# Kernel optimization log

Measured on AMD Instinct MI355X. Metric: run time of the kernel, lower is better.

The kernel has to match this reference:

```python
import jax, jax.numpy as jnp
import numpy as np

D_MODEL = 1024
N_HEADS = 16
D_K = D_MODEL // N_HEADS
B, L = 2, 2048


def setup_inputs() -> dict:
    key = jax.random.key(0)
    ks = jax.random.split(key, 13)
    s = 0.02
    inp = {
        'query': jax.random.normal(ks[0], (B, L, D_MODEL), jnp.float32),
        'key': jax.random.normal(ks[1], (B, L, D_MODEL), jnp.float32),
        'value': jax.random.normal(ks[2], (B, L, D_MODEL), jnp.float32),
        'mask': jax.random.randint(ks[3], (1, 1, L, L), 0, 2).astype(bool),
        'W_q': jax.random.normal(ks[4], (D_MODEL, D_MODEL), jnp.float32) * s,
        'b_q': jnp.zeros((D_MODEL,), jnp.float32),
        'W_k': jax.random.normal(ks[5], (D_MODEL, D_MODEL), jnp.float32) * s,
        'b_k': jnp.zeros((D_MODEL,), jnp.float32),
        'W_v': jax.random.normal(ks[6], (D_MODEL, D_MODEL), jnp.float32) * s,
        'b_v': jnp.zeros((D_MODEL,), jnp.float32),
        'W_o': jax.random.normal(ks[7], (D_MODEL, D_MODEL), jnp.float32) * s,
        'b_o': jnp.zeros((D_MODEL,), jnp.float32),
    }
    return inp


def _split_heads(x):
    b, l, _ = x.shape
    return x.reshape(b, l, N_HEADS, D_K).transpose(0, 2, 1, 3)  # [B,H,L,dk]


def reference(query, key, value, mask, W_q, b_q, W_k, b_k, W_v, b_v, W_o, b_o):
    q = _split_heads(query @ W_q + b_q)
    k = _split_heads(key @ W_k + b_k)
    v = _split_heads(value @ W_v + b_v)
    # Unscaled attention logits [B,H,L,L] (NO 1/sqrt(dk))
    logits = jnp.einsum('bhqd,bhkd->bhqk', q, k)
    logits = jnp.where(mask, -jnp.inf, logits)
    w = jax.nn.softmax(logits, axis=-1)
    w = jnp.nan_to_num(w, nan=0.0)  # fully-masked rows -> zeros
    attended = jnp.einsum('bhqk,bhkd->bhqd', w, v)
    # dropout in eval mode = identity; combine heads
    out = attended.transpose(0, 2, 1, 3).reshape(B, L, D_MODEL)
    return out @ W_o + b_o
```

## Files before the change

### kernel.cpp

```cpp
#include <hip/hip_runtime.h>
#include <hip/hip_bf16.h>
#include <stdint.h>


typedef __bf16 bf16;
typedef __bf16 bf16x8 __attribute__((ext_vector_type(8)));
typedef float f32x4 __attribute__((ext_vector_type(4)));

#define AS1 __attribute__((address_space(1)))
#define AS3 __attribute__((address_space(3)))

__device__ __forceinline__ void g2l16(const void* g, void* l) {
    __builtin_amdgcn_global_load_lds((AS1 void*)g, (AS3 void*)l, 16, 0, 0);
}

__global__ __launch_bounds__(256) void cvt3_kernel(const float* __restrict__ a0,
                                                   const float* __restrict__ a1,
                                                   const float* __restrict__ a2,
                                                   bf16* o0, bf16* o1, bf16* o2) {
    int y = blockIdx.y;
    const float* in = (y == 0) ? a0 : (y == 1) ? a1 : a2;
    bf16* out = (y == 0) ? o0 : (y == 1) ? o1 : o2;
    int idx = blockIdx.x * 256 + threadIdx.x;
    float4 v = ((const float4*)in)[idx];
    __align__(8) bf16 o[4];
    o[0] = (bf16)v.x; o[1] = (bf16)v.y; o[2] = (bf16)v.z; o[3] = (bf16)v.w;
    *(uint2*)(out + (size_t)idx * 4) = *(const uint2*)o;
}

__global__ __launch_bounds__(256) void mdetect_kernel(const unsigned int* __restrict__ w,
                                                      int* __restrict__ flag) {
    int idx = blockIdx.x * 256 + threadIdx.x;
    unsigned v = w[idx];
    int f = 0;
    if (v == 0x3F800000u) f = 2;
    else if (v > 1u) f = 1;
    unsigned long long b1 = __ballot(f & 1);
    unsigned long long b2 = __ballot(f & 2);
    if ((threadIdx.x & 63) == 0) {
        int agg = (b1 ? 1 : 0) | (b2 ? 2 : 0);
        if (agg) atomicOr(flag, agg);
    }
}

__global__ __launch_bounds__(256) void mpack_kernel(const void* __restrict__ mask,
                                                    unsigned long long* __restrict__ mb,
                                                    const int* __restrict__ flag) {
    int idx = blockIdx.x * 256 + threadIdx.x;
    int f = *flag;
    bool v;
    if (f & 2)      v = ((const float*)mask)[idx] != 0.0f;
    else if (f & 1) v = ((const unsigned char*)mask)[idx] != 0;
    else            v = ((const int*)mask)[idx] != 0;
    unsigned long long b = __ballot(v);
    if ((threadIdx.x & 63) == 0) mb[idx >> 6] = b;
}

__global__ __launch_bounds__(256) void wtrans_kernel(const float* W0, const float* W1,
                                                     const float* W2, const float* W3,
                                                     bf16* T0, bf16* T1, bf16* T2, bf16* T3) {
    const float* W; bf16* T;
    int y = blockIdx.y;
    if (y == 0)      { W = W0; T = T0; }
    else if (y == 1) { W = W1; T = T1; }
    else if (y == 2) { W = W2; T = T2; }
    else             { W = W3; T = T3; }
    int tx = blockIdx.x & 15, ty = blockIdx.x >> 4;
    int n0 = tx * 64, k0 = ty * 64;
    __shared__ __align__(16) bf16 t[64 * 72];
    int tid = threadIdx.x;
    #pragma unroll
    for (int rr = 0; rr < 4; ++rr) {
        int idx = rr * 256 + tid;
        int r = idx >> 4, c4 = (idx & 15) * 4;
        float4 v = *(const float4*)(W + (size_t)(k0 + r) * 1024 + n0 + c4);
        __align__(8) bf16 o[4];
        o[0] = (bf16)v.x; o[1] = (bf16)v.y; o[2] = (bf16)v.z; o[3] = (bf16)v.w;
        *(uint2*)&t[r * 72 + c4] = *(const uint2*)o;
    }
    __syncthreads();
    #pragma unroll
    for (int rr = 0; rr < 2; ++rr) {
        int idx = rr * 256 + tid;
        int n = idx >> 3, kc = (idx & 7) * 8;
        __align__(16) bf16 o[8];
        #pragma unroll
        for (int j = 0; j < 8; ++j) o[j] = t[(kc + j) * 72 + n];
        *(uint4*)(T + (size_t)(n0 + n) * 1024 + k0 + kc) = *(const uint4*)o;
    }
}

template <int MODE>
__device__ __forceinline__ void gemm128_core(const bf16* __restrict__ A,
                                             const bf16* __restrict__ Bt,
                                             const float* __restrict__ bias,
                                             void* __restrict__ Out, int bm, int bn) {
    __shared__ __align__(16) bf16 la[128 * 32];
    __shared__ __align__(16) bf16 lb[128 * 32];
    int tid = threadIdx.x;
    int w = tid >> 6, lane = tid & 63;
    int quad = lane >> 4, col = lane & 15;
    int wm = w >> 1, wn = w & 1;
    int m0 = bm * 128, n0 = bn * 128;
    f32x4 acc[4][4];
    f32x4 z = {0.f, 0.f, 0.f, 0.f};
    #pragma unroll
    for (int i = 0; i < 4; ++i)
        #pragma unroll
        for (int j = 0; j < 4; ++j) acc[i][j] = z;
    int srow = lane >> 2;
    int skc = (lane & 3) * 8;
    for (int kt = 0; kt < 32; ++kt) {
        int kk = kt * 32;
        __syncthreads();
        #pragma unroll
        for (int rr = 0; rr < 2; ++rr) {
            int ch = rr * 4 + w;
            int row = ch * 16 + srow;
            g2l16(A + (size_t)(m0 + row) * 1024 + kk + skc, &la[ch * 512]);
            g2l16(Bt + (size_t)(n0 + row) * 1024 + kk + skc, &lb[ch * 512]);
        }
        __syncthreads();
        bf16x8 af[4], bfr[4];
        #pragma unroll
        for (int mt = 0; mt < 4; ++mt)
            af[mt] = *(const bf16x8*)&la[(wm * 64 + mt * 16 + col) * 32 + quad * 8];
        #pragma unroll
        for (int nt = 0; nt < 4; ++nt)
            bfr[nt] = *(const bf16x8*)&lb[(wn * 64 + nt * 16 + col) * 32 + quad * 8];
        #pragma unroll
        for (int mt = 0; mt < 4; ++mt)
            #pragma unroll
            for (int nt = 0; nt < 4; ++nt)
                acc[mt][nt] = __builtin_amdgcn_mfma_f32_16x16x32_bf16(
                    af[mt], bfr[nt], acc[mt][nt], 0, 0, 0);
    }
    float bia[4];
    #pragma unroll
    for (int nt = 0; nt < 4; ++nt) bia[nt] = bias[n0 + wn * 64 + nt * 16 + col];
    #pragma unroll
    for (int mt = 0; mt < 4; ++mt) {
        #pragma unroll
        for (int nt = 0; nt < 4; ++nt) {
            #pragma unroll
            for (int r = 0; r < 4; ++r) {
                int m = m0 + wm * 64 + mt * 16 + quad * 4 + r;
                int n = n0 + wn * 64 + nt * 16 + col;
                float v = acc[mt][nt][r] + bia[nt];
                if (MODE == 0) {
                    int b = m >> 11, l = m & 2047, h = n >> 6, d = n & 63;
                    ((bf16*)Out)[(((size_t)b * 16 + h) * 2048 + l) * 64 + d] = (bf16)v;
                } else if (MODE == 1) {
                    ((float*)Out)[(size_t)m * 1024 + n] = v;
                } else {
                    int b = m >> 11, l = m & 2047, h = n >> 6, d = n & 63;
                    ((bf16*)Out)[(((size_t)b * 16 + h) * 64 + d) * 2048 + l] = (bf16)v;
                }
            }
        }
    }
}

__global__ __launch_bounds__(256) void qk_kernel(
    const bf16* Xq, const bf16* Xk, const bf16* Wq, const bf16* Wk,
    const float* bq, const float* bk, bf16* Qh, bf16* Kh) {
    int y = blockIdx.y;
    const bf16* A = y ? Xk : Xq;
    const bf16* Bt = y ? Wk : Wq;
    const float* bi = y ? bk : bq;
    bf16* O = y ? Kh : Qh;
    gemm128_core<0>(A, Bt, bi, O, blockIdx.x >> 3, blockIdx.x & 7);
}

__global__ __launch_bounds__(256) void vproj_kernel(const bf16* Xv, const bf16* Wv,
                                                    const float* bv, bf16* Vt) {
    gemm128_core<2>(Xv, Wv, bv, Vt, blockIdx.x >> 3, blockIdx.x & 7);
}

__global__ __launch_bounds__(256) void ogemm_kernel(const bf16* A, const bf16* Wt,
                                                    const float* bias, float* Out) {
    gemm128_core<1>(A, Wt, bias, Out, blockIdx.x >> 3, blockIdx.x & 7);
}

__global__ __launch_bounds__(256) void attn_kernel(const bf16* __restrict__ Qh,
                                                   const bf16* __restrict__ Kh,
                                                   const bf16* __restrict__ Vt,
                                                   const unsigned long long* __restrict__ mb,
                                                   bf16* __restrict__ att) {
    int bh = blockIdx.x, qt = blockIdx.y;
    int b = bh >> 4, h = bh & 15;
    int q0 = qt * 64;
    __shared__ __align__(16) bf16 qs[64 * 64];
    __shared__ __align__(16) bf16 ks[64 * 64];
    __shared__ __align__(16) bf16 vs[64 * 64];
    __shared__ __align__(16) bf16 ps[4 * 16 * 72];
    int tid = threadIdx.x;
    int w = tid >> 6, lane = tid & 63;
    int quad = lane >> 4, col = lane & 15;
    int c7 = col & 7;
    int sr = lane >> 3;
    int sg = (lane & 7) ^ (sr & 7);
    int swz0 = (quad ^ c7) * 8;
    int swz1 = ((4 + quad) ^ c7) * 8;

    #pragma unroll
    for (int rr = 0; rr < 2; ++rr) {
        int ch = rr * 4 + w;
        int r = ch * 8 + sr;
        g2l16(Qh + ((size_t)bh * 2048 + q0 + r) * 64 + sg * 8, &qs[ch * 512]);
    }
    __syncthreads();
    bf16x8 aq[2];
    aq[0] = *(const bf16x8*)&qs[(w * 16 + col) * 64 + swz0];
    aq[1] = *(const bf16x8*)&qs[(w * 16 + col) * 64 + swz1];

    f32x4 O[4];
    f32x4 z = {0.f, 0.f, 0.f, 0.f};
    float rs[4] = {0.f, 0.f, 0.f, 0.f};
    #pragma unroll
    for (int dt = 0; dt < 4; ++dt) O[dt] = z;

    for (int kt = 0; kt < 32; ++kt) {
        __syncthreads();
        #pragma unroll
        for (int rr = 0; rr < 2; ++rr) {
            int ch = rr * 4 + w;
            int r = ch * 8 + sr;
            g2l16(Kh + ((size_t)bh * 2048 + kt * 64 + r) * 64 + sg * 8, &ks[ch * 512]);
            g2l16(Vt + ((size_t)bh * 64 + r) * 2048 + kt * 64 + sg * 8, &vs[ch * 512]);
        }
        __syncthreads();

        f32x4 s[4];
        #pragma unroll
        for (int nt = 0; nt < 4; ++nt) {
            s[nt] = z;
            bf16x8 bk0 = *(const bf16x8*)&ks[(nt * 16 + col) * 64 + swz0];
            s[nt] = __builtin_amdgcn_mfma_f32_16x16x32_bf16(aq[0], bk0, s[nt], 0, 0, 0);
            bf16x8 bk1 = *(const bf16x8*)&ks[(nt * 16 + col) * 64 + swz1];
            s[nt] = __builtin_amdgcn_mfma_f32_16x16x32_bf16(aq[1], bk1, s[nt], 0, 0, 0);
        }

        #pragma unroll
        for (int r = 0; r < 4; ++r) {
            unsigned long long t = mb[(size_t)(q0 + w * 16 + quad * 4 + r) * 32 + kt] >> col;
            #pragma unroll
            for (int nt = 0; nt < 4; ++nt) {
                float p = __expf(s[nt][r] - 12.0f);
                if ((t >> (nt * 16)) & 1ull) p = 0.0f;
                rs[r] += p;
                s[nt][r] = p;
            }
        }

        #pragma unroll
        for (int nt = 0; nt < 4; ++nt)
            #pragma unroll
            for (int r = 0; r < 4; ++r)
                ps[w * 1152 + (quad * 4 + r) * 72 + nt * 16 + col] = (bf16)s[nt][r];

        bf16x8 ap[2];
        ap[0] = *(const bf16x8*)&ps[w * 1152 + col * 72 + quad * 8];
        ap[1] = *(const bf16x8*)&ps[w * 1152 + col * 72 + 32 + quad * 8];
        #pragma unroll
        for (int dt = 0; dt < 4; ++dt) {
            bf16x8 bv0 = *(const bf16x8*)&vs[(dt * 16 + col) * 64 + swz0];
            O[dt] = __builtin_amdgcn_mfma_f32_16x16x32_bf16(ap[0], bv0, O[dt], 0, 0, 0);
            bf16x8 bv1 = *(const bf16x8*)&vs[(dt * 16 + col) * 64 + swz1];
            O[dt] = __builtin_amdgcn_mfma_f32_16x16x32_bf16(ap[1], bv1, O[dt], 0, 0, 0);
        }
    }

    #pragma unroll
    for (int r = 0; r < 4; ++r) {
        #pragma unroll
        for (int d = 1; d < 16; d <<= 1) rs[r] += __shfl_xor(rs[r], d);
    }

    #pragma unroll
    for (int r = 0; r < 4; ++r) {
        float inv = (rs[r] > 0.f) ? 1.0f / rs[r] : 0.f;
        int qg = q0 + w * 16 + quad * 4 + r;
        #pragma unroll
        for (int dt = 0; dt < 4; ++dt) {
            float ov = O[dt][r] * inv;
            att[((size_t)b * 2048 + qg) * 1024 + h * 64 + dt * 16 + col] = (bf16)ov;
        }
    }
}

extern "C" void kernel_launch(void* const* d_in, const int* in_sizes, int n_in,
                              void* d_out, int out_size, void* d_ws, size_t ws_size,
                              hipStream_t stream) {
    (void)in_sizes; (void)n_in; (void)out_size; (void)ws_size;
    const float* query = (const float*)d_in[0];
    const float* key_  = (const float*)d_in[1];
    const float* value = (const float*)d_in[2];
    const void*  mask  = d_in[3];
    const float* W_q = (const float*)d_in[4];
    const float* b_q = (const float*)d_in[5];
    const float* W_k = (const float*)d_in[6];
    const float* b_k = (const float*)d_in[7];
    const float* W_v = (const float*)d_in[8];
    const float* b_v = (const float*)d_in[9];
    const float* W_o = (const float*)d_in[10];
    const float* b_o = (const float*)d_in[11];

    char* ws = (char*)d_ws;
    bf16* Xq  = (bf16*)(ws + 0);
    bf16* Xk  = (bf16*)(ws + 8388608);
    bf16* Xv  = (bf16*)(ws + 16777216);
    bf16* Wtq = (bf16*)(ws + 25165824);
    bf16* Wtk = (bf16*)(ws + 27262976);
    bf16* Wtv = (bf16*)(ws + 29360128);
    bf16* Wto = (bf16*)(ws + 31457280);
    bf16* Qh  = (bf16*)(ws + 33554432);
    bf16* Kh  = (bf16*)(ws + 41943040);
    bf16* Vt  = (bf16*)(ws + 50331648);
    bf16* att = (bf16*)(ws + 58720256);
    unsigned long long* mb = (unsigned long long*)(ws + 67108864);
    int* flag = (int*)(ws + 67633152);

    hipMemsetAsync(flag, 0, 4, stream);
    mdetect_kernel<<<4096, 256, 0, stream>>>((const unsigned int*)mask, flag);
    mpack_kernel<<<16384, 256, 0, stream>>>(mask, mb, flag);

    cvt3_kernel<<<dim3(4096, 3), 256, 0, stream>>>(query, key_, value, Xq, Xk, Xv);
    wtrans_kernel<<<dim3(256, 4), 256, 0, stream>>>(W_q, W_k, W_v, W_o, Wtq, Wtk, Wtv, Wto);

    qk_kernel<<<dim3(256, 2), 256, 0, stream>>>(Xq, Xk, Wtq, Wtk, b_q, b_k, Qh, Kh);
    vproj_kernel<<<256, 256, 0, stream>>>(Xv, Wtv, b_v, Vt);
    attn_kernel<<<dim3(32, 32), 256, 0, stream>>>(Qh, Kh, Vt, mb, att);
    ogemm_kernel<<<256, 256, 0, stream>>>(att, Wto, b_o, (float*)d_out);
}
```

Measured before the change: 295.8 us.

## Enlarge attention query tile, fuse QKV projections, exp2 softmax, smaller output-GEMM tiles

Each attention block now covers 128 query rows instead of 64, with two 16-row MFMA tiles per wave. Every K/V tile loaded into LDS is therefore reused across twice as many queries, at the cost of more registers and LDS. Q is pre-scaled by log2(e) in the projection epilogue, so the softmax uses exp2 directly and the constant -12 shift is dropped. The Q, K and V projections are merged into one launch, and the output GEMM gets its own 64x128 tile kernel that runs twice as many blocks.

New measurement: 274.4 us. 7.3% less time.

```diff
diff --git a/kernel.cpp b/kernel.cpp
--- a/kernel.cpp
+++ b/kernel.cpp
@@ -13,6 +13,8 @@
 __device__ __forceinline__ void g2l16(const void* g, void* l) {
     __builtin_amdgcn_global_load_lds((AS1 void*)g, (AS3 void*)l, 16, 0, 0);
 }
+
+#define LOG2E 1.44269504088896f
 
 __global__ __launch_bounds__(256) void cvt3_kernel(const float* __restrict__ a0,
                                                    const float* __restrict__ a1,
@@ -94,7 +96,8 @@
 __device__ __forceinline__ void gemm128_core(const bf16* __restrict__ A,
                                              const bf16* __restrict__ Bt,
                                              const float* __restrict__ bias,
-                                             void* __restrict__ Out, int bm, int bn) {
+                                             void* __restrict__ Out, int bm, int bn,
+                                             float scale) {
     __shared__ __align__(16) bf16 la[128 * 32];
     __shared__ __align__(16) bf16 lb[128 * 32];
     int tid = threadIdx.x;
@@ -146,12 +149,10 @@
             for (int r = 0; r < 4; ++r) {
                 int m = m0 + wm * 64 + mt * 16 + quad * 4 + r;
                 int n = n0 + wn * 64 + nt * 16 + col;
-                float v = acc[mt][nt][r] + bia[nt];
+                float v = (acc[mt][nt][r] + bia[nt]) * scale;
                 if (MODE == 0) {
                     int b = m >> 11, l = m & 2047, h = n >> 6, d = n & 63;
                     ((bf16*)Out)[(((size_t)b * 16 + h) * 2048 + l) * 64 + d] = (bf16)v;
-                } else if (MODE == 1) {
-                    ((float*)Out)[(size_t)m * 1024 + n] = v;
                 } else {
                     int b = m >> 11, l = m & 2047, h = n >> 6, d = n & 63;
                     ((bf16*)Out)[(((size_t)b * 16 + h) * 64 + d) * 2048 + l] = (bf16)v;
@@ -161,25 +162,70 @@
     }
 }
 
-__global__ __launch_bounds__(256) void qk_kernel(
-    const bf16* Xq, const bf16* Xk, const bf16* Wq, const bf16* Wk,
-    const float* bq, const float* bk, bf16* Qh, bf16* Kh) {
+__global__ __launch_bounds__(256) void qkv_kernel(
+    const bf16* Xq, const bf16* Xk, const bf16* Xv,
+    const bf16* Wq, const bf16* Wk, const bf16* Wv,
+    const float* bq, const float* bk, const float* bv,
+    bf16* Qh, bf16* Kh, bf16* Vt) {
     int y = blockIdx.y;
-    const bf16* A = y ? Xk : Xq;
-    const bf16* Bt = y ? Wk : Wq;
-    const float* bi = y ? bk : bq;
-    bf16* O = y ? Kh : Qh;
-    gemm128_core<0>(A, Bt, bi, O, blockIdx.x >> 3, blockIdx.x & 7);
-}
-
-__global__ __launch_bounds__(256) void vproj_kernel(const bf16* Xv, const bf16* Wv,
-                                                    const float* bv, bf16* Vt) {
-    gemm128_core<2>(Xv, Wv, bv, Vt, blockIdx.x >> 3, blockIdx.x & 7);
-}
-
-__global__ __launch_bounds__(256) void ogemm_kernel(const bf16* A, const bf16* Wt,
-                                                    const float* bias, float* Out) {
-    gemm128_core<1>(A, Wt, bias, Out, blockIdx.x >> 3, blockIdx.x & 7);
+    int bm = blockIdx.x >> 3, bn = blockIdx.x & 7;
+    if (y == 0)      gemm128_core<0>(Xq, Wq, bq, Qh, bm, bn, LOG2E);
+    else if (y == 1) gemm128_core<0>(Xk, Wk, bk, Kh, bm, bn, 1.0f);
+    else             gemm128_core<2>(Xv, Wv, bv, Vt, bm, bn, 1.0f);
+}
+
+__global__ __launch_bounds__(256) void ogemm_kernel(const bf16* __restrict__ A,
+                                                    const bf16* __restrict__ Wt,
+                                                    const float* __restrict__ bias,
+                                                    float* __restrict__ Out) {
+    int bm = blockIdx.x >> 3, bn = blockIdx.x & 7;
+    __shared__ __align__(16) bf16 la[64 * 32];
+    __shared__ __align__(16) bf16 lb[128 * 32];
+    int tid = threadIdx.x;
+    int w = tid >> 6, lane = tid & 63;
+    int quad = lane >> 4, col = lane & 15;
+    int m0 = bm * 64, n0 = bn * 128;
+    f32x4 acc[4][2];
+    f32x4 z = {0.f, 0.f, 0.f, 0.f};
+    #pragma unroll
+    for (int i = 0; i < 4; ++i) { acc[i][0] = z; acc[i][1] = z; }
+    int srow = lane >> 2;
+    int skc = (lane & 3) * 8;
+    for (int kt = 0; kt < 32; ++kt) {
+        int kk = kt * 32;
+        __syncthreads();
+        g2l16(A + (size_t)(m0 + w * 16 + srow) * 1024 + kk + skc, &la[w * 512]);
+        #pragma unroll
+        for (int rr = 0; rr < 2; ++rr) {
+            int ch = rr * 4 + w;
+            g2l16(Wt + (size_t)(n0 + ch * 16 + srow) * 1024 + kk + skc, &lb[ch * 512]);
+        }
+        __syncthreads();
+        bf16x8 af[4], bfr[2];
+        #pragma unroll
+        for (int mt = 0; mt < 4; ++mt)
+            af[mt] = *(const bf16x8*)&la[(mt * 16 + col) * 32 + quad * 8];
+        #pragma unroll
+        for (int nt = 0; nt < 2; ++nt)
+            bfr[nt] = *(const bf16x8*)&lb[(w * 32 + nt * 16 + col) * 32 + quad * 8];
+        #pragma unroll
+        for (int mt = 0; mt < 4; ++mt)
+            #pragma unroll
+            for (int nt = 0; nt < 2; ++nt)
+                acc[mt][nt] = __builtin_amdgcn_mfma_f32_16x16x32_bf16(
+                    af[mt], bfr[nt], acc[mt][nt], 0, 0, 0);
+    }
+    float bia[2];
+    bia[0] = bias[n0 + w * 32 + col];
+    bia[1] = bias[n0 + w * 32 + 16 + col];
+    #pragma unroll
+    for (int mt = 0; mt < 4; ++mt)
+        #pragma unroll
+        for (int nt = 0; nt < 2; ++nt)
+            #pragma unroll
+            for (int r = 0; r < 4; ++r)
+                Out[(size_t)(m0 + mt * 16 + quad * 4 + r) * 1024 +
+                    n0 + w * 32 + nt * 16 + col] = acc[mt][nt][r] + bia[nt];
 }
 
 __global__ __launch_bounds__(256) void attn_kernel(const bf16* __restrict__ Qh,
@@ -189,36 +235,40 @@
                                                    bf16* __restrict__ att) {
     int bh = blockIdx.x, qt = blockIdx.y;
     int b = bh >> 4, h = bh & 15;
-    int q0 = qt * 64;
-    __shared__ __align__(16) bf16 qs[64 * 64];
+    int q0 = qt * 128;
+    __shared__ __align__(16) bf16 qs[128 * 64];
     __shared__ __align__(16) bf16 ks[64 * 64];
     __shared__ __align__(16) bf16 vs[64 * 64];
-    __shared__ __align__(16) bf16 ps[4 * 16 * 72];
+    __shared__ __align__(16) bf16 ps[4 * 32 * 72];
     int tid = threadIdx.x;
     int w = tid >> 6, lane = tid & 63;
     int quad = lane >> 4, col = lane & 15;
     int c7 = col & 7;
     int sr = lane >> 3;
-    int sg = (lane & 7) ^ (sr & 7);
+    int sg = (lane & 7) ^ sr;
     int swz0 = (quad ^ c7) * 8;
     int swz1 = ((4 + quad) ^ c7) * 8;
 
     #pragma unroll
-    for (int rr = 0; rr < 2; ++rr) {
-        int ch = rr * 4 + w;
-        int r = ch * 8 + sr;
-        g2l16(Qh + ((size_t)bh * 2048 + q0 + r) * 64 + sg * 8, &qs[ch * 512]);
+    for (int i = 0; i < 4; ++i) {
+        int ch = w * 4 + i;
+        g2l16(Qh + ((size_t)bh * 2048 + q0 + ch * 8 + sr) * 64 + sg * 8, &qs[ch * 512]);
     }
     __syncthreads();
-    bf16x8 aq[2];
-    aq[0] = *(const bf16x8*)&qs[(w * 16 + col) * 64 + swz0];
-    aq[1] = *(const bf16x8*)&qs[(w * 16 + col) * 64 + swz1];
-
-    f32x4 O[4];
+    bf16x8 aq[2][2];
+    #pragma unroll
+    for (int mt = 0; mt < 2; ++mt) {
+        aq[mt][0] = *(const bf16x8*)&qs[(w * 32 + mt * 16 + col) * 64 + swz0];
+        aq[mt][1] = *(const bf16x8*)&qs[(w * 32 + mt * 16 + col) * 64 + swz1];
+    }
+
     f32x4 z = {0.f, 0.f, 0.f, 0.f};
-    float rs[4] = {0.f, 0.f, 0.f, 0.f};
-    #pragma unroll
-    for (int dt = 0; dt < 4; ++dt) O[dt] = z;
+    f32x4 O[2][4];
+    float rs[2][4];
+    #pragma unroll
+    for (int mt = 0; mt < 2; ++mt)
+        #pragma unroll
+        for (int i = 0; i < 4; ++i) { O[mt][i] = z; rs[mt][i] = 0.f; }
 
     for (int kt = 0; kt < 32; ++kt) {
         __syncthreads();
@@ -231,60 +281,69 @@
         }
         __syncthreads();
 
-        f32x4 s[4];
+        f32x4 s[2][4];
         #pragma unroll
         for (int nt = 0; nt < 4; ++nt) {
-            s[nt] = z;
+            s[0][nt] = z; s[1][nt] = z;
             bf16x8 bk0 = *(const bf16x8*)&ks[(nt * 16 + col) * 64 + swz0];
-            s[nt] = __builtin_amdgcn_mfma_f32_16x16x32_bf16(aq[0], bk0, s[nt], 0, 0, 0);
+            s[0][nt] = __builtin_amdgcn_mfma_f32_16x16x32_bf16(aq[0][0], bk0, s[0][nt], 0, 0, 0);
+            s[1][nt] = __builtin_amdgcn_mfma_f32_16x16x32_bf16(aq[1][0], bk0, s[1][nt], 0, 0, 0);
             bf16x8 bk1 = *(const bf16x8*)&ks[(nt * 16 + col) * 64 + swz1];
-            s[nt] = __builtin_amdgcn_mfma_f32_16x16x32_bf16(aq[1], bk1, s[nt], 0, 0, 0);
-        }
-
-        #pragma unroll
-        for (int r = 0; r < 4; ++r) {
-            unsigned long long t = mb[(size_t)(q0 + w * 16 + quad * 4 + r) * 32 + kt] >> col;
-            #pragma unroll
-            for (int nt = 0; nt < 4; ++nt) {
-                float p = __expf(s[nt][r] - 12.0f);
-                if ((t >> (nt * 16)) & 1ull) p = 0.0f;
-                rs[r] += p;
-                s[nt][r] = p;
+            s[0][nt] = __builtin_amdgcn_mfma_f32_16x16x32_bf16(aq[0][1], bk1, s[0][nt], 0, 0, 0);
+            s[1][nt] = __builtin_amdgcn_mfma_f32_16x16x32_bf16(aq[1][1], bk1, s[1][nt], 0, 0, 0);
+        }
+
+        #pragma unroll
+        for (int mt = 0; mt < 2; ++mt) {
+            #pragma unroll
+            for (int r = 0; r < 4; ++r) {
+                unsigned long long t =
+                    mb[(size_t)(q0 + w * 32 + mt * 16 + quad * 4 + r) * 32 + kt] >> col;
+                #pragma unroll
+                for (int nt = 0; nt < 4; ++nt) {
+                    float p = __builtin_amdgcn_exp2f(s[mt][nt][r]);
+                    if ((t >> (nt * 16)) & 1ull) p = 0.0f;
+                    rs[mt][r] += p;
+                    ps[w * 2304 + (mt * 16 + quad * 4 + r) * 72 + nt * 16 + col] = (bf16)p;
+                }
             }
         }
 
-        #pragma unroll
-        for (int nt = 0; nt < 4; ++nt)
-            #pragma unroll
-            for (int r = 0; r < 4; ++r)
-                ps[w * 1152 + (quad * 4 + r) * 72 + nt * 16 + col] = (bf16)s[nt][r];
-
-        bf16x8 ap[2];
-        ap[0] = *(const bf16x8*)&ps[w * 1152 + col * 72 + quad * 8];
-        ap[1] = *(const bf16x8*)&ps[w * 1152 + col * 72 + 32 + quad * 8];
+        bf16x8 ap[2][2];
+        #pragma unroll
+        for (int mt = 0; mt < 2; ++mt) {
+            ap[mt][0] = *(const bf16x8*)&ps[w * 2304 + (mt * 16 + col) * 72 + quad * 8];
+            ap[mt][1] = *(const bf16x8*)&ps[w * 2304 + (mt * 16 + col) * 72 + 32 + quad * 8];
+        }
         #pragma unroll
         for (int dt = 0; dt < 4; ++dt) {
             bf16x8 bv0 = *(const bf16x8*)&vs[(dt * 16 + col) * 64 + swz0];
-            O[dt] = __builtin_amdgcn_mfma_f32_16x16x32_bf16(ap[0], bv0, O[dt], 0, 0, 0);
+            O[0][dt] = __builtin_amdgcn_mfma_f32_16x16x32_bf16(ap[0][0], bv0, O[0][dt], 0, 0, 0);
+            O[1][dt] = __builtin_amdgcn_mfma_f32_16x16x32_bf16(ap[1][0], bv0, O[1][dt], 0, 0, 0);
             bf16x8 bv1 = *(const bf16x8*)&vs[(dt * 16 + col) * 64 + swz1];
-            O[dt] = __builtin_amdgcn_mfma_f32_16x16x32_bf16(ap[1], bv1, O[dt], 0, 0, 0);
-        }
-    }
-
-    #pragma unroll
-    for (int r = 0; r < 4; ++r) {
-        #pragma unroll
-        for (int d = 1; d < 16; d <<= 1) rs[r] += __shfl_xor(rs[r], d);
-    }
-
-    #pragma unroll
-    for (int r = 0; r < 4; ++r) {
-        float inv = (rs[r] > 0.f) ? 1.0f / rs[r] : 0.f;
-        int qg = q0 + w * 16 + quad * 4 + r;
-        #pragma unroll
-        for (int dt = 0; dt < 4; ++dt) {
-            float ov = O[dt][r] * inv;
-            att[((size_t)b * 2048 + qg) * 1024 + h * 64 + dt * 16 + col] = (bf16)ov;
+            O[0][dt] = __builtin_amdgcn_mfma_f32_16x16x32_bf16(ap[0][1], bv1, O[0][dt], 0, 0, 0);
+            O[1][dt] = __builtin_amdgcn_mfma_f32_16x16x32_bf16(ap[1][1], bv1, O[1][dt], 0, 0, 0);
+        }
+    }
+
+    #pragma unroll
+    for (int mt = 0; mt < 2; ++mt)
+        #pragma unroll
+        for (int r = 0; r < 4; ++r)
+            #pragma unroll
+            for (int d = 1; d < 16; d <<= 1) rs[mt][r] += __shfl_xor(rs[mt][r], d);
+
+    #pragma unroll
+    for (int mt = 0; mt < 2; ++mt) {
+        #pragma unroll
+        for (int r = 0; r < 4; ++r) {
+            float inv = (rs[mt][r] > 0.f) ? 1.0f / rs[mt][r] : 0.f;
+            int qg = q0 + w * 32 + mt * 16 + quad * 4 + r;
+            #pragma unroll
+            for (int dt = 0; dt < 4; ++dt) {
+                float ov = O[mt][dt][r] * inv;
+                att[((size_t)b * 2048 + qg) * 1024 + h * 64 + dt * 16 + col] = (bf16)ov;
+            }
         }
     }
 }
@@ -328,8 +387,8 @@
     cvt3_kernel<<<dim3(4096, 3), 256, 0, stream>>>(query, key_, value, Xq, Xk, Xv);
     wtrans_kernel<<<dim3(256, 4), 256, 0, stream>>>(W_q, W_k, W_v, W_o, Wtq, Wtk, Wtv, Wto);
 
-    qk_kernel<<<dim3(256, 2), 256, 0, stream>>>(Xq, Xk, Wtq, Wtk, b_q, b_k, Qh, Kh);
-    vproj_kernel<<<256, 256, 0, stream>>>(Xv, Wtv, b_v, Vt);
-    attn_kernel<<<dim3(32, 32), 256, 0, stream>>>(Qh, Kh, Vt, mb, att);
-    ogemm_kernel<<<256, 256, 0, stream>>>(att, Wto, b_o, (float*)d_out);
-}
+    qkv_kernel<<<dim3(256, 3), 256, 0, stream>>>(Xq, Xk, Xv, Wtq, Wtk, Wtv,
+                                                 b_q, b_k, b_v, Qh, Kh, Vt);
+    attn_kernel<<<dim3(32, 16), 256, 0, stream>>>(Qh, Kh, Vt, mb, att);
+    ogemm_kernel<<<512, 256, 0, stream>>>(att, Wto, b_o, (float*)d_out);
+}
```
